# Optimization experiments

Measured on AMD Instinct MI355X. Metric: run time of the kernel, lower is better.

## Reference

```python
import jax, jax.numpy as jnp
import numpy as np

DIM = 1024
HEADS = 16


def setup_inputs() -> dict:
    key = jax.random.key(0)
    k1, k2, k3, k4 = jax.random.split(key, 4)
    X = jax.random.normal(k1, (4, 2048, DIM), dtype=jnp.float32)
    # torch Linear weight is [out, in]; store transposed [in, out] for x @ W
    W_qkv = jax.random.normal(k2, (DIM, 3 * DIM), dtype=jnp.float32) * (DIM ** -0.5)
    W_out = jax.random.normal(k3, (DIM, DIM), dtype=jnp.float32) * (DIM ** -0.5)
    b_out = jax.random.normal(k4, (DIM,), dtype=jnp.float32) * 0.01
    return {"X": X, "W_qkv": W_qkv, "W_out": W_out, "b_out": b_out}


def reference(X, W_qkv, W_out, b_out):
    b, t, d = X.shape
    h = HEADS
    hd = d // h
    scale = d ** -0.5  # NOTE: scales by full dim, matching the original module
    qkv = X @ W_qkv  # [b, t, 3d]
    q, k, v = jnp.split(qkv, 3, axis=-1)
    # [b, t, d] -> [b, h, t, hd]
    def to_heads(x):
        return x.reshape(b, t, h, hd).transpose(0, 2, 1, 3)
    q, k, v = to_heads(q), to_heads(k), to_heads(v)
    dots = jnp.einsum('bhid,bhjd->bhij', q, k) * scale  # [b, h, t, t]
    attn = jax.nn.softmax(dots, axis=-1)
    out = jnp.einsum('bhij,bhjd->bhid', attn, v)  # [b, h, t, hd]
    out = out.transpose(0, 2, 1, 3).reshape(b, t, d)
    return out @ W_out + b_out
```

## Files before the change

### kernel.cpp

```cpp
#include <hip/hip_runtime.h>
#include <hip/hip_bf16.h>
#include <stdint.h>

#define DIMD 1024
#define NB 4
#define NT 2048
#define NH 16
#define BT (NB*NT)
#define NQKV (3*DIMD)

typedef __attribute__((ext_vector_type(8))) __bf16 bf16x8;
typedef __attribute__((ext_vector_type(4))) __bf16 bf16x4;
typedef __attribute__((ext_vector_type(4))) float f32x4;
typedef __attribute__((ext_vector_type(16))) float f32x16;

#define MFMA16(a,b,c) __builtin_amdgcn_mfma_f32_16x16x32_bf16((a),(b),(c),0,0,0)
#define MFMA32(a,b,c) __builtin_amdgcn_mfma_f32_32x32x16_bf16((a),(b),(c),0,0,0)

#define QSCALE 0.0450842200277801f

__device__ __forceinline__ void gld16(const void* g, void* l) {
  __builtin_amdgcn_global_load_lds((const __attribute__((address_space(1))) void*)g,
                                   (__attribute__((address_space(3))) void*)l,
                                   16, 0, 0);
}

__device__ __forceinline__ unsigned pkbf(float a, float b) {
  unsigned short ua = __builtin_bit_cast(unsigned short, (__bf16)a);
  unsigned short ub = __builtin_bit_cast(unsigned short, (__bf16)b);
  return (unsigned)ua | ((unsigned)ub << 16);
}

__global__ __launch_bounds__(256) void k_cvt(const float* __restrict__ in,
                                             __bf16* __restrict__ out, int n4) {
  int i = blockIdx.x * blockDim.x + threadIdx.x;
  int st = gridDim.x * blockDim.x;
  for (; i < n4; i += st) {
    float4 v = ((const float4*)in)[i];
    bf16x4 o;
    o[0] = (__bf16)v.x; o[1] = (__bf16)v.y; o[2] = (__bf16)v.z; o[3] = (__bf16)v.w;
    ((bf16x4*)out)[i] = o;
  }
}

__global__ __launch_bounds__(256) void k_tcvt(const float* __restrict__ in,
                                              __bf16* __restrict__ out, int K, int N) {
  __shared__ __bf16 t[64][72];
  int n0 = blockIdx.x * 64, k0 = blockIdx.y * 64;
  int r = threadIdx.x >> 2, c0 = (threadIdx.x & 3) * 16;
  const float4* src = (const float4*)(in + (size_t)(k0 + r) * N + n0 + c0);
#pragma unroll
  for (int i = 0; i < 4; ++i) {
    float4 v = src[i];
    t[r][c0 + i*4 + 0] = (__bf16)v.x;
    t[r][c0 + i*4 + 1] = (__bf16)v.y;
    t[r][c0 + i*4 + 2] = (__bf16)v.z;
    t[r][c0 + i*4 + 3] = (__bf16)v.w;
  }
  __syncthreads();
  bf16x8 o0, o1;
#pragma unroll
  for (int i = 0; i < 8; ++i) o0[i] = t[c0 + i][r];
#pragma unroll
  for (int i = 0; i < 8; ++i) o1[i] = t[c0 + 8 + i][r];
  __bf16* dst = out + (size_t)(n0 + r) * K + k0 + c0;
  *(bf16x8*)dst = o0;
  *(bf16x8*)(dst + 8) = o1;
}

template<int MODE>
__global__ __launch_bounds__(256) void k_gemm(const __bf16* __restrict__ A,
                                              const __bf16* __restrict__ Bt,
                                              int M, int N, int K,
                                              __bf16* __restrict__ oQK,
                                              __bf16* __restrict__ oVt,
                                              float* __restrict__ oF,
                                              const float* __restrict__ bias) {
  __shared__ alignas(16) __bf16 As[128 * 32];
  __shared__ alignas(16) __bf16 Bs[128 * 32];
  const int tid = threadIdx.x;
  const int lane = tid & 63, w = tid >> 6;
  const int lr = lane & 15, lo = lane >> 4;
  const int wm = w >> 1, wn = w & 1;
  const int m0 = blockIdx.y * 128, n0 = blockIdx.x * 128;
  const __bf16* Ab = A + (size_t)m0 * K;
  const __bf16* Bb = Bt + (size_t)n0 * K;
  f32x4 acc[4][4] = {};
  const int s0i = tid, s1i = 256 + tid;

  for (int k0 = 0; k0 < K; k0 += 32) {
    gld16(Ab + (size_t)(s0i >> 2) * K + k0 + (s0i & 3) * 8, (char*)As + s0i * 16);
    gld16(Ab + (size_t)(s1i >> 2) * K + k0 + (s1i & 3) * 8, (char*)As + s1i * 16);
    gld16(Bb + (size_t)(s0i >> 2) * K + k0 + (s0i & 3) * 8, (char*)Bs + s0i * 16);
    gld16(Bb + (size_t)(s1i >> 2) * K + k0 + (s1i & 3) * 8, (char*)Bs + s1i * 16);
    asm volatile("s_waitcnt vmcnt(0)" ::: "memory");
    __syncthreads();
    bf16x8 af[4], bfr[4];
#pragma unroll
    for (int mt = 0; mt < 4; ++mt)
      af[mt] = *(const bf16x8*)(As + (wm*64 + mt*16 + lr) * 32 + lo * 8);
#pragma unroll
    for (int nt = 0; nt < 4; ++nt)
      bfr[nt] = *(const bf16x8*)(Bs + (wn*64 + nt*16 + lr) * 32 + lo * 8);
#pragma unroll
    for (int mt = 0; mt < 4; ++mt)
#pragma unroll
      for (int nt = 0; nt < 4; ++nt)
        acc[mt][nt] = MFMA16(af[mt], bfr[nt], acc[mt][nt]);
    __syncthreads();
  }

  if (MODE == 0) {
    const int cb = n0 + wn * 64;
    if (cb < 2048) {
      const float f = (cb < 1024) ? QSCALE : 1.0f;
#pragma unroll
      for (int mt = 0; mt < 4; ++mt)
#pragma unroll
        for (int nt = 0; nt < 4; ++nt) {
          int col = cb + nt * 16 + lr;
          int mrow = m0 + wm * 64 + mt * 16 + lo * 4;
#pragma unroll
          for (int r = 0; r < 4; ++r)
            oQK[(size_t)(mrow + r) * 2048 + col] = (__bf16)(acc[mt][nt][r] * f);
        }
    } else {
#pragma unroll
      for (int mt = 0; mt < 4; ++mt)
#pragma unroll
        for (int nt = 0; nt < 4; ++nt) {
          int dd = cb - 2048 + nt * 16 + lr;
          int mrow = m0 + wm * 64 + mt * 16 + lo * 4;
          int bb = mrow >> 11, tt = mrow & 2047;
          bf16x4 pk;
#pragma unroll
          for (int r = 0; r < 4; ++r) pk[r] = (__bf16)acc[mt][nt][r];
          *(bf16x4*)(oVt + ((size_t)(bb << 10) + dd) * 2048 + tt) = pk;
        }
    }
  } else {
#pragma unroll
    for (int mt = 0; mt < 4; ++mt)
#pragma unroll
      for (int nt = 0; nt < 4; ++nt) {
        int col = n0 + wn * 64 + nt * 16 + lr;
        float bv = bias[col];
        int mrow = m0 + wm * 64 + mt * 16 + lo * 4;
#pragma unroll
        for (int r = 0; r < 4; ++r)
          oF[(size_t)(mrow + r) * N + col] = acc[mt][nt][r] + bv;
      }
  }
}

__global__ __launch_bounds__(256) void k_attn(const __bf16* __restrict__ QK,
                                              const __bf16* __restrict__ Vt,
                                              __bf16* __restrict__ AO) {
  __shared__ alignas(16) __bf16 Ks[2][64 * 72];
  __shared__ alignas(16) __bf16 Vs[2][64 * 72];
  const int tid = threadIdx.x, w = tid >> 6, lane = tid & 63;
  const int l31 = lane & 31, hi = lane >> 5;
  const int P = blockIdx.x;
  const int low3 = P & 7, g = P >> 3;
  const int qc = g & 15;
  const int bh = ((g >> 4) << 3) + low3;
  const int h = bh & 15, b = bh >> 4;
  const int q0 = qc * 128 + w * 32;

  bf16x8 qf[4];
  {
    const __bf16* Qb = QK + (size_t)(b * 2048 + q0 + l31) * 2048 + h * 64 + hi * 8;
#pragma unroll
    for (int dc = 0; dc < 4; ++dc) qf[dc] = *(const bf16x8*)(Qb + dc * 16);
  }
  const __bf16* Kg = QK + (size_t)(b * 2048) * 2048 + 1024 + h * 64;
  const __bf16* Vg = Vt + (size_t)(b * 1024 + h * 64) * 2048;

  const int i0 = tid, i1 = 256 + tid, i2 = 512 + tid;
  int r0 = i0 / 9, c0 = i0 - r0 * 9; c0 = (c0 == 8) ? 0 : c0;
  int r1 = i1 / 9, c1 = i1 - r1 * 9; c1 = (c1 == 8) ? 0 : c1;
  int r2 = i2 / 9, c2 = i2 - r2 * 9; c2 = (c2 == 8) ? 0 : c2;
  const __bf16* kP0 = Kg + (size_t)r0 * 2048 + c0 * 8;
  const __bf16* kP1 = Kg + (size_t)r1 * 2048 + c1 * 8;
  const __bf16* kP2 = Kg + (size_t)r2 * 2048 + c2 * 8;
  const __bf16* vP0 = Vg + (size_t)r0 * 2048 + c0 * 8;
  const __bf16* vP1 = Vg + (size_t)r1 * 2048 + c1 * 8;
  const __bf16* vP2 = Vg + (size_t)r2 * 2048 + c2 * 8;

  f32x16 o0 = {0,0,0,0,0,0,0,0,0,0,0,0,0,0,0,0};
  f32x16 o1 = {0,0,0,0,0,0,0,0,0,0,0,0,0,0,0,0};
  float ln = 0.f;

  auto STAGE = [&](int x) {
    char* bK = (char*)&Ks[x][0];
    char* bV = (char*)&Vs[x][0];
    gld16(kP0, bK + i0 * 16);
    gld16(vP0, bV + i0 * 16);
    gld16(kP1, bK + i1 * 16);
    gld16(vP1, bV + i1 * 16);
    if (tid < 64) {
      gld16(kP2, bK + i2 * 16);
      gld16(vP2, bV + i2 * 16);
    }
    kP0 += 64 * 2048; kP1 += 64 * 2048; kP2 += 64 * 2048;
    vP0 += 64; vP1 += 64; vP2 += 64;
  };

  STAGE(0);
  asm volatile("s_waitcnt vmcnt(0)" ::: "memory");
  __syncthreads();

  int x = 0;
#pragma unroll 2
  for (int t = 0; t < 32; ++t) {
    if (t < 31) STAGE(x ^ 1);
    const __bf16* Kl = &Ks[x][0];
    const __bf16* Vl = &Vs[x][0];

    f32x16 s0 = {0,0,0,0,0,0,0,0,0,0,0,0,0,0,0,0};
    f32x16 s1 = {0,0,0,0,0,0,0,0,0,0,0,0,0,0,0,0};
    {
      bf16x8 kf[4];
#pragma unroll
      for (int dc = 0; dc < 4; ++dc)
        kf[dc] = *(const bf16x8*)(Kl + l31 * 72 + dc * 16 + hi * 8);
      __builtin_amdgcn_s_setprio(1);
#pragma unroll
      for (int dc = 0; dc < 4; ++dc) s0 = MFMA32(kf[dc], qf[dc], s0);
      __builtin_amdgcn_s_setprio(0);
#pragma unroll
      for (int dc = 0; dc < 4; ++dc)
        kf[dc] = *(const bf16x8*)(Kl + (32 + l31) * 72 + dc * 16 + hi * 8);
      __builtin_amdgcn_s_setprio(1);
#pragma unroll
      for (int dc = 0; dc < 4; ++dc) s1 = MFMA32(kf[dc], qf[dc], s1);
      __builtin_amdgcn_s_setprio(0);
    }

    float p0a[16], p1a[16];
#pragma unroll
    for (int r = 0; r < 16; ++r) {
      p0a[r] = __builtin_amdgcn_exp2f(s0[r]);
      p1a[r] = __builtin_amdgcn_exp2f(s1[r]);
    }
    float sA = 0.f, sB = 0.f, sC = 0.f, sD = 0.f;
#pragma unroll
    for (int r = 0; r < 4; ++r) {
      sA += p0a[r];      sB += p0a[4 + r];
      sC += p0a[8 + r];  sD += p0a[12 + r];
      sA += p1a[r];      sB += p1a[4 + r];
      sC += p1a[8 + r];  sD += p1a[12 + r];
    }
    ln += (sA + sB) + (sC + sD);

    unsigned pw[4][4];
#pragma unroll
    for (int c = 0; c < 4; ++c) {
      const float* pp = (c < 2) ? p0a : p1a;
      const int rb = (c & 1) * 8;
      unsigned A01 = pkbf(pp[rb + 0], pp[rb + 1]);
      unsigned A23 = pkbf(pp[rb + 2], pp[rb + 3]);
      unsigned A45 = pkbf(pp[rb + 4], pp[rb + 5]);
      unsigned A67 = pkbf(pp[rb + 6], pp[rb + 7]);
      asm("v_permlane32_swap_b32 %0, %1" : "+v"(A01), "+v"(A45));
      asm("v_permlane32_swap_b32 %0, %1" : "+v"(A23), "+v"(A67));
      pw[c][0] = A01; pw[c][1] = A23; pw[c][2] = A45; pw[c][3] = A67;
    }

    {
      bf16x8 vf[4];
#pragma unroll
      for (int c = 0; c < 4; ++c)
        vf[c] = *(const bf16x8*)(Vl + l31 * 72 + c * 16 + hi * 8);
      __builtin_amdgcn_s_setprio(1);
#pragma unroll
      for (int c = 0; c < 4; ++c) {
        union { unsigned u[4]; bf16x8 v; } pc;
        pc.u[0] = pw[c][0]; pc.u[1] = pw[c][1]; pc.u[2] = pw[c][2]; pc.u[3] = pw[c][3];
        o0 = MFMA32(pc.v, vf[c], o0);
      }
      __builtin_amdgcn_s_setprio(0);
#pragma unroll
      for (int c = 0; c < 4; ++c)
        vf[c] = *(const bf16x8*)(Vl + (32 + l31) * 72 + c * 16 + hi * 8);
      __builtin_amdgcn_s_setprio(1);
#pragma unroll
      for (int c = 0; c < 4; ++c) {
        union { unsigned u[4]; bf16x8 v; } pc;
        pc.u[0] = pw[c][0]; pc.u[1] = pw[c][1]; pc.u[2] = pw[c][2]; pc.u[3] = pw[c][3];
        o1 = MFMA32(pc.v, vf[c], o1);
      }
      __builtin_amdgcn_s_setprio(0);
    }

    asm volatile("s_waitcnt vmcnt(0)" ::: "memory");
    __syncthreads();
    x ^= 1;
  }

  float lnt = ln + __shfl_xor(ln, 32, 64);
  float inv = 1.0f / lnt;
  __bf16* Ob = AO + (size_t)(b * 2048 + q0) * 1024 + h * 64;
#pragma unroll
  for (int r = 0; r < 16; ++r) {
    int qr = (r & 3) + 8 * (r >> 2) + 4 * hi;
    float iv = __shfl(inv, qr, 64);
    Ob[(size_t)qr * 1024 + l31] = (__bf16)(o0[r] * iv);
    Ob[(size_t)qr * 1024 + 32 + l31] = (__bf16)(o1[r] * iv);
  }
}

extern "C" void kernel_launch(void* const* d_in, const int* in_sizes, int n_in,
                              void* d_out, int out_size, void* d_ws, size_t ws_size,
                              hipStream_t stream) {
  const float* X    = (const float*)d_in[0];
  const float* Wqkv = (const float*)d_in[1];
  const float* Wout = (const float*)d_in[2];
  const float* bout = (const float*)d_in[3];
  float* out = (float*)d_out;
  char* ws = (char*)d_ws;

  __bf16* Xb  = (__bf16*)(ws);
  __bf16* Wqt = (__bf16*)(ws + 16777216);
  __bf16* Wot = (__bf16*)(ws + 23068672);
  __bf16* QKb = (__bf16*)(ws + 25165824);
  __bf16* Vtb = (__bf16*)(ws + 58720256);
  __bf16* AOb = (__bf16*)(ws + 75497472);

  k_cvt<<<2048, 256, 0, stream>>>(X, Xb, (BT * DIMD) / 4);
  k_tcvt<<<dim3(NQKV / 64, DIMD / 64), 256, 0, stream>>>(Wqkv, Wqt, DIMD, NQKV);
  k_tcvt<<<dim3(DIMD / 64, DIMD / 64), 256, 0, stream>>>(Wout, Wot, DIMD, DIMD);
  k_gemm<0><<<dim3(NQKV / 128, BT / 128), 256, 0, stream>>>(
      Xb, Wqt, BT, NQKV, DIMD, QKb, Vtb, nullptr, nullptr);
  k_attn<<<1024, 256, 0, stream>>>(QKb, Vtb, AOb);
  k_gemm<1><<<dim3(DIMD / 128, BT / 128), 256, 0, stream>>>(
      AOb, Wot, BT, DIMD, DIMD, nullptr, nullptr, out, bout);
}
```

Before: 223.8 us.

## Process 64 query rows per wave in attention to reuse K/V fragments

Each wave in the attention kernel now handles two 32-row query blocks instead of one, so every K and V fragment loaded from LDS feeds twice as many MFMAs. The grid is halved to 512 blocks of 256 queries, and launch bounds request two blocks per CU. This cuts LDS read traffic and global K/V staging per query. The cost is many more accumulator and probability registers, which can lower occupancy, and fewer blocks to spread across the 256 CUs.

```diff
diff --git a/kernel.cpp b/kernel.cpp
--- a/kernel.cpp
+++ b/kernel.cpp
@@ -153,25 +153,28 @@
   }
 }
 
-__global__ __launch_bounds__(256) void k_attn(const __bf16* __restrict__ QK,
-                                              const __bf16* __restrict__ Vt,
-                                              __bf16* __restrict__ AO) {
+__global__ __launch_bounds__(256, 2) void k_attn(const __bf16* __restrict__ QK,
+                                                 const __bf16* __restrict__ Vt,
+                                                 __bf16* __restrict__ AO) {
   __shared__ alignas(16) __bf16 Ks[2][64 * 72];
   __shared__ alignas(16) __bf16 Vs[2][64 * 72];
   const int tid = threadIdx.x, w = tid >> 6, lane = tid & 63;
   const int l31 = lane & 31, hi = lane >> 5;
   const int P = blockIdx.x;
   const int low3 = P & 7, g = P >> 3;
-  const int qc = g & 15;
-  const int bh = ((g >> 4) << 3) + low3;
+  const int qc = g & 7;
+  const int bh = ((g >> 3) << 3) + low3;
   const int h = bh & 15, b = bh >> 4;
-  const int q0 = qc * 128 + w * 32;
-
-  bf16x8 qf[4];
+  const int q0 = qc * 256 + w * 64;
+
+  bf16x8 qfA[4], qfB[4];
   {
     const __bf16* Qb = QK + (size_t)(b * 2048 + q0 + l31) * 2048 + h * 64 + hi * 8;
 #pragma unroll
-    for (int dc = 0; dc < 4; ++dc) qf[dc] = *(const bf16x8*)(Qb + dc * 16);
+    for (int dc = 0; dc < 4; ++dc) qfA[dc] = *(const bf16x8*)(Qb + dc * 16);
+    Qb += (size_t)32 * 2048;
+#pragma unroll
+    for (int dc = 0; dc < 4; ++dc) qfB[dc] = *(const bf16x8*)(Qb + dc * 16);
   }
   const __bf16* Kg = QK + (size_t)(b * 2048) * 2048 + 1024 + h * 64;
   const __bf16* Vg = Vt + (size_t)(b * 1024 + h * 64) * 2048;
@@ -187,9 +190,11 @@
   const __bf16* vP1 = Vg + (size_t)r1 * 2048 + c1 * 8;
   const __bf16* vP2 = Vg + (size_t)r2 * 2048 + c2 * 8;
 
-  f32x16 o0 = {0,0,0,0,0,0,0,0,0,0,0,0,0,0,0,0};
-  f32x16 o1 = {0,0,0,0,0,0,0,0,0,0,0,0,0,0,0,0};
-  float ln = 0.f;
+  f32x16 oA0 = {0,0,0,0,0,0,0,0,0,0,0,0,0,0,0,0};
+  f32x16 oA1 = {0,0,0,0,0,0,0,0,0,0,0,0,0,0,0,0};
+  f32x16 oB0 = {0,0,0,0,0,0,0,0,0,0,0,0,0,0,0,0};
+  f32x16 oB1 = {0,0,0,0,0,0,0,0,0,0,0,0,0,0,0,0};
+  float lnA = 0.f, lnB = 0.f;
 
   auto STAGE = [&](int x) {
     char* bK = (char*)&Ks[x][0];
@@ -206,37 +211,7 @@
     vP0 += 64; vP1 += 64; vP2 += 64;
   };
 
-  STAGE(0);
-  asm volatile("s_waitcnt vmcnt(0)" ::: "memory");
-  __syncthreads();
-
-  int x = 0;
-#pragma unroll 2
-  for (int t = 0; t < 32; ++t) {
-    if (t < 31) STAGE(x ^ 1);
-    const __bf16* Kl = &Ks[x][0];
-    const __bf16* Vl = &Vs[x][0];
-
-    f32x16 s0 = {0,0,0,0,0,0,0,0,0,0,0,0,0,0,0,0};
-    f32x16 s1 = {0,0,0,0,0,0,0,0,0,0,0,0,0,0,0,0};
-    {
-      bf16x8 kf[4];
-#pragma unroll
-      for (int dc = 0; dc < 4; ++dc)
-        kf[dc] = *(const bf16x8*)(Kl + l31 * 72 + dc * 16 + hi * 8);
-      __builtin_amdgcn_s_setprio(1);
-#pragma unroll
-      for (int dc = 0; dc < 4; ++dc) s0 = MFMA32(kf[dc], qf[dc], s0);
-      __builtin_amdgcn_s_setprio(0);
-#pragma unroll
-      for (int dc = 0; dc < 4; ++dc)
-        kf[dc] = *(const bf16x8*)(Kl + (32 + l31) * 72 + dc * 16 + hi * 8);
-      __builtin_amdgcn_s_setprio(1);
-#pragma unroll
-      for (int dc = 0; dc < 4; ++dc) s1 = MFMA32(kf[dc], qf[dc], s1);
-      __builtin_amdgcn_s_setprio(0);
-    }
-
+  auto SMPACK = [&](const f32x16& s0, const f32x16& s1, unsigned pw[4][4], float& ln) {
     float p0a[16], p1a[16];
 #pragma unroll
     for (int r = 0; r < 16; ++r) {
@@ -252,8 +227,6 @@
       sC += p1a[8 + r];  sD += p1a[12 + r];
     }
     ln += (sA + sB) + (sC + sD);
-
-    unsigned pw[4][4];
 #pragma unroll
     for (int c = 0; c < 4; ++c) {
       const float* pp = (c < 2) ? p0a : p1a;
@@ -266,29 +239,64 @@
       asm("v_permlane32_swap_b32 %0, %1" : "+v"(A23), "+v"(A67));
       pw[c][0] = A01; pw[c][1] = A23; pw[c][2] = A45; pw[c][3] = A67;
     }
-
+  };
+
+  STAGE(0);
+  asm volatile("s_waitcnt vmcnt(0)" ::: "memory");
+  __syncthreads();
+
+  int x = 0;
+#pragma unroll 2
+  for (int t = 0; t < 32; ++t) {
+    if (t < 31) STAGE(x ^ 1);
+    const __bf16* Kl = &Ks[x][0];
+    const __bf16* Vl = &Vs[x][0];
+
+    f32x16 sA0 = {0,0,0,0,0,0,0,0,0,0,0,0,0,0,0,0};
+    f32x16 sA1 = {0,0,0,0,0,0,0,0,0,0,0,0,0,0,0,0};
+    f32x16 sB0 = {0,0,0,0,0,0,0,0,0,0,0,0,0,0,0,0};
+    f32x16 sB1 = {0,0,0,0,0,0,0,0,0,0,0,0,0,0,0,0};
     {
-      bf16x8 vf[4];
+      bf16x8 kf[8];
+#pragma unroll
+      for (int dc = 0; dc < 4; ++dc)
+        kf[dc] = *(const bf16x8*)(Kl + l31 * 72 + dc * 16 + hi * 8);
+#pragma unroll
+      for (int dc = 0; dc < 4; ++dc)
+        kf[4 + dc] = *(const bf16x8*)(Kl + (32 + l31) * 72 + dc * 16 + hi * 8);
+      __builtin_amdgcn_s_setprio(1);
+#pragma unroll
+      for (int dc = 0; dc < 4; ++dc) {
+        sA0 = MFMA32(kf[dc], qfA[dc], sA0);
+        sB0 = MFMA32(kf[dc], qfB[dc], sB0);
+        sA1 = MFMA32(kf[4 + dc], qfA[dc], sA1);
+        sB1 = MFMA32(kf[4 + dc], qfB[dc], sB1);
+      }
+      __builtin_amdgcn_s_setprio(0);
+    }
+
+    unsigned pwA[4][4], pwB[4][4];
+    SMPACK(sA0, sA1, pwA, lnA);
+    SMPACK(sB0, sB1, pwB, lnB);
+
+    {
+      bf16x8 vf[8];
 #pragma unroll
       for (int c = 0; c < 4; ++c)
         vf[c] = *(const bf16x8*)(Vl + l31 * 72 + c * 16 + hi * 8);
+#pragma unroll
+      for (int c = 0; c < 4; ++c)
+        vf[4 + c] = *(const bf16x8*)(Vl + (32 + l31) * 72 + c * 16 + hi * 8);
       __builtin_amdgcn_s_setprio(1);
 #pragma unroll
       for (int c = 0; c < 4; ++c) {
-        union { unsigned u[4]; bf16x8 v; } pc;
-        pc.u[0] = pw[c][0]; pc.u[1] = pw[c][1]; pc.u[2] = pw[c][2]; pc.u[3] = pw[c][3];
-        o0 = MFMA32(pc.v, vf[c], o0);
-      }
-      __builtin_amdgcn_s_setprio(0);
-#pragma unroll
-      for (int c = 0; c < 4; ++c)
-        vf[c] = *(const bf16x8*)(Vl + (32 + l31) * 72 + c * 16 + hi * 8);
-      __builtin_amdgcn_s_setprio(1);
-#pragma unroll
-      for (int c = 0; c < 4; ++c) {
-        union { unsigned u[4]; bf16x8 v; } pc;
-        pc.u[0] = pw[c][0]; pc.u[1] = pw[c][1]; pc.u[2] = pw[c][2]; pc.u[3] = pw[c][3];
-        o1 = MFMA32(pc.v, vf[c], o1);
+        union { unsigned u[4]; bf16x8 v; } pa, pb;
+        pa.u[0] = pwA[c][0]; pa.u[1] = pwA[c][1]; pa.u[2] = pwA[c][2]; pa.u[3] = pwA[c][3];
+        pb.u[0] = pwB[c][0]; pb.u[1] = pwB[c][1]; pb.u[2] = pwB[c][2]; pb.u[3] = pwB[c][3];
+        oA0 = MFMA32(pa.v, vf[c], oA0);
+        oB0 = MFMA32(pb.v, vf[c], oB0);
+        oA1 = MFMA32(pa.v, vf[4 + c], oA1);
+        oB1 = MFMA32(pb.v, vf[4 + c], oB1);
       }
       __builtin_amdgcn_s_setprio(0);
     }
@@ -298,15 +306,19 @@
     x ^= 1;
   }
 
-  float lnt = ln + __shfl_xor(ln, 32, 64);
-  float inv = 1.0f / lnt;
+  float lA = lnA + __shfl_xor(lnA, 32, 64);
+  float lB = lnB + __shfl_xor(lnB, 32, 64);
+  float invA = 1.0f / lA, invB = 1.0f / lB;
   __bf16* Ob = AO + (size_t)(b * 2048 + q0) * 1024 + h * 64;
 #pragma unroll
   for (int r = 0; r < 16; ++r) {
     int qr = (r & 3) + 8 * (r >> 2) + 4 * hi;
-    float iv = __shfl(inv, qr, 64);
-    Ob[(size_t)qr * 1024 + l31] = (__bf16)(o0[r] * iv);
-    Ob[(size_t)qr * 1024 + 32 + l31] = (__bf16)(o1[r] * iv);
+    float ivA = __shfl(invA, qr, 64);
+    float ivB = __shfl(invB, qr, 64);
+    Ob[(size_t)qr * 1024 + l31] = (__bf16)(oA0[r] * ivA);
+    Ob[(size_t)qr * 1024 + 32 + l31] = (__bf16)(oA1[r] * ivA);
+    Ob[(size_t)(32 + qr) * 1024 + l31] = (__bf16)(oB0[r] * ivB);
+    Ob[(size_t)(32 + qr) * 1024 + 32 + l31] = (__bf16)(oB1[r] * ivB);
   }
 }
 
@@ -332,7 +344,7 @@
   k_tcvt<<<dim3(DIMD / 64, DIMD / 64), 256, 0, stream>>>(Wout, Wot, DIMD, DIMD);
   k_gemm<0><<<dim3(NQKV / 128, BT / 128), 256, 0, stream>>>(
       Xb, Wqt, BT, NQKV, DIMD, QKb, Vtb, nullptr, nullptr);
-  k_attn<<<1024, 256, 0, stream>>>(QKb, Vtb, AOb);
+  k_attn<<<512, 256, 0, stream>>>(QKb, Vtb, AOb);
   k_gemm<1><<<dim3(DIMD / 128, BT / 128), 256, 0, stream>>>(
       AOb, Wot, BT, DIMD, DIMD, nullptr, nullptr, out, bout);
 }
```

Result: faster. 207.3 us (-7.4%).
